# Optimization experiments

Measured on AMD Instinct MI355X. Metric: run time of the kernel, lower is better.

The kernel has to match this reference:

```python
import jax, jax.numpy as jnp
import numpy as np

N = 100000      # nodes
E = 1600000     # edges
F_IN = 512      # num_features
H = 128         # hidden
C = 40          # num_classes
K = 10          # Chebyshev order


def setup_inputs() -> dict:
    key = jax.random.key(0)
    ks = jax.random.split(key, 6)
    x = jax.random.normal(ks[0], (N, F_IN), dtype=jnp.float32)
    edge_index = jax.random.randint(ks[1], (2, E), 0, N, dtype=jnp.int32)
    W1 = jax.random.normal(ks[2], (F_IN, H), dtype=jnp.float32) / np.sqrt(F_IN).astype(np.float32)
    b1 = jnp.zeros((H,), dtype=jnp.float32)
    W2 = jax.random.normal(ks[3], (H, C), dtype=jnp.float32) / np.sqrt(H).astype(np.float32)
    b2 = jnp.zeros((C,), dtype=jnp.float32)
    # Chebyshev coefficients temp[K+1]
    temp = 1.0 + 0.1 * jax.random.normal(ks[4], (K + 1,), dtype=jnp.float32)
    return {"x": x, "edge_index": edge_index, "W1": W1, "b1": b1, "W2": W2, "b2": b2, "temp": temp}


def reference(x, edge_index, W1, b1, W2, b2, temp):
    # MLP encoder (eval mode: dropout is identity)
    h = jax.nn.relu(x @ W1 + b1)          # [N, H]
    h = h @ W2 + b2                        # [N, C]

    # gcn_norm: add self-loops, symmetric normalization
    self_loop = jnp.arange(N, dtype=edge_index.dtype)
    row = jnp.concatenate([edge_index[0], self_loop])   # [E+N]
    col = jnp.concatenate([edge_index[1], self_loop])
    deg = jax.ops.segment_sum(jnp.ones_like(row, dtype=jnp.float32), row, num_segments=N)
    dis = jnp.where(deg > 0, jax.lax.rsqrt(jnp.maximum(deg, 1.0)), 0.0)
    norm = dis[row] * dis[col]             # [E+N]

    def prop(v):  # A_hat @ v : gather-scale-scatter over edges
        return jax.ops.segment_sum(norm[:, None] * v[col], row, num_segments=N)

    # Chebyshev recurrence: Tx_k = 2*A_hat*Tx_{k-1} - Tx_{k-2}
    Tx0 = h
    Tx1 = prop(h)
    out0 = temp[0] * Tx0 + temp[1] * Tx1

    def body(carry, coe):
        t0, t1, acc = carry
        t2 = 2.0 * prop(t1) - t0
        return (t1, t2, acc + coe * t2), None

    (_, _, out), _ = jax.lax.scan(body, (Tx0, Tx1, out0), temp[2:])
    return jax.nn.log_softmax(out, axis=1)
```

## Files before the change

### kernel.cpp

```cpp
#include <hip/hip_runtime.h>
#include <hip/hip_bf16.h>
#include <cstdint>
#include <cstddef>

#define NN   100000
#define EE   1600000
#define FIN  512
#define HID  128
#define CC   40
#define KORD 10
#define SHB  80
#define SHSTRIDE ((size_t)NN * SHB)

typedef __attribute__((ext_vector_type(4))) float f4;
typedef __attribute__((ext_vector_type(8))) short short8_t;
typedef __attribute__((ext_vector_type(4))) unsigned int u4;
typedef __attribute__((ext_vector_type(4), aligned(4))) int i4u;

__device__ __forceinline__ unsigned short cvt_bf16(float f) {
  union { float f; unsigned u; } a; a.f = f;
  unsigned r = a.u + 0x7fffu + ((a.u >> 16) & 1u);
  return (unsigned short)(r >> 16);
}
__device__ __forceinline__ unsigned pk_bf(float a, float b) {
  union { float f; unsigned u; } x, y; x.f = a; y.f = b;
  unsigned ra = x.u + 0x7fffu + ((x.u >> 16) & 1u);
  unsigned rb = y.u + 0x7fffu + ((y.u >> 16) & 1u);
  return (ra >> 16) | (rb & 0xffff0000u);
}
__device__ __forceinline__ unsigned pk_tr(float a, float b) {
  union { float f; unsigned u; } x, y; x.f = a; y.f = b;
  return (x.u >> 16) | (y.u & 0xffff0000u);
}
__device__ __forceinline__ f4 cvf2(unsigned lo, unsigned hi) {
  union { unsigned u; float f; } a, b, c, d;
  a.u = lo << 16; b.u = lo & 0xffff0000u;
  c.u = hi << 16; d.u = hi & 0xffff0000u;
  f4 r; r.x = a.f; r.y = b.f; r.z = c.f; r.w = d.f; return r;
}

__global__ __launch_bounds__(256) void k_dw(const int* __restrict__ rowI, int* __restrict__ deg,
                                            const float* __restrict__ W1, unsigned short* __restrict__ W1T,
                                            int ndeg) {
  int b = blockIdx.x;
  if (b < ndeg) {
    int i = b * 256 + threadIdx.x;
    if (i < EE) atomicAdd(&deg[rowI[i]], 1);
  } else {
    int idx = (b - ndeg) * 256 + threadIdx.x;
    int k = idx >> 7, n = idx & 127;
    W1T[(k >> 5) * 4096 + n * 32 + (k & 31)] = cvt_bf16(W1[idx]);
  }
}

__global__ __launch_bounds__(256) void k_scan1(const int* __restrict__ cnt, int* __restrict__ excl,
                                               int* __restrict__ bsums) {
  __shared__ int s[256];
  int tid = threadIdx.x;
  int base = blockIdx.x * 1024 + tid * 4;
  int v0 = (base + 0 < NN) ? cnt[base + 0] + 1 : 0;
  int v1 = (base + 1 < NN) ? cnt[base + 1] + 1 : 0;
  int v2 = (base + 2 < NN) ? cnt[base + 2] + 1 : 0;
  int v3 = (base + 3 < NN) ? cnt[base + 3] + 1 : 0;
  int tsum = v0 + v1 + v2 + v3;
  s[tid] = tsum;
  __syncthreads();
  for (int off = 1; off < 256; off <<= 1) {
    int t = (tid >= off) ? s[tid - off] : 0;
    __syncthreads();
    if (tid >= off) s[tid] += t;
    __syncthreads();
  }
  int run = s[tid] - tsum;
  if (tid == 255) bsums[blockIdx.x] = s[255];
  if (base + 0 < NN) excl[base + 0] = run; run += v0;
  if (base + 1 < NN) excl[base + 1] = run; run += v1;
  if (base + 2 < NN) excl[base + 2] = run; run += v2;
  if (base + 3 < NN) excl[base + 3] = run;
}

__global__ __launch_bounds__(128) void k_scan2(int* __restrict__ bsums, int nb) {
  __shared__ int s[128];
  int tid = threadIdx.x;
  int v = (tid < nb) ? bsums[tid] : 0;
  s[tid] = v;
  __syncthreads();
  for (int off = 1; off < 128; off <<= 1) {
    int t = (tid >= off) ? s[tid - off] : 0;
    __syncthreads();
    if (tid >= off) s[tid] += t;
    __syncthreads();
  }
  if (tid < nb) bsums[tid] = s[tid] - v;
}

__global__ __launch_bounds__(256) void k_scan3(const int* __restrict__ cnt, int* __restrict__ rs,
                                               int* __restrict__ cur, const int* __restrict__ bsums,
                                               float* __restrict__ dis, float* __restrict__ sqd,
                                               float* __restrict__ invd) {
  int i = blockIdx.x * 256 + threadIdx.x;
  if (i < NN) {
    int v = rs[i] + bsums[i >> 10];
    rs[i] = v;
    cur[i] = v;
    int d = cnt[i] + 1;
    if (i == NN - 1) rs[NN] = v + d;
    float fd = (float)d;
    dis[i]  = rsqrtf(fd);
    sqd[i]  = sqrtf(fd);
    invd[i] = 1.0f / fd;
  }
}

#define SLICE_ROWS (NN / 8)
#define SC_CHUNK   2048
__global__ __launch_bounds__(256) void k_scatter(const int* __restrict__ rowI, const int* __restrict__ colI,
                                                 int* __restrict__ cur, int* __restrict__ colS) {
  int slice = blockIdx.x & 7;
  int chunk = blockIdx.x >> 3;
  int lo = slice * SLICE_ROWS, hi = lo + SLICE_ROWS;
#pragma unroll
  for (int t = 0; t < SC_CHUNK / 256; ++t) {
    int i = chunk * SC_CHUNK + t * 256 + threadIdx.x;
    if (i < EE + NN) {
      int r = (i < EE) ? rowI[i] : (i - EE);
      if (r >= lo && r < hi) {
        int c = (i < EE) ? colI[i] : r;
        int pos = atomicAdd(&cur[r], 1);
        colS[pos] = c * SHB;
      }
    }
  }
}

#define LDK 40
__global__ __launch_bounds__(256) void k_gemm1(const float* __restrict__ x, const unsigned short* __restrict__ W1T,
                                               const float* __restrict__ b1, float* __restrict__ h1) {
  __shared__ __align__(16) float As_f[128 * 32];
  __shared__ __align__(16) short Bs_s[128][LDK];
  int tid  = threadIdx.x;
  int wave = tid >> 6, lane = tid & 63;
  int blockRow = blockIdx.x * 128;
  int wr = (wave & 1) * 64, wc = (wave >> 1) * 64;
  int l15 = lane & 15, hi4 = lane >> 4;

  int sr = (wave << 5) + (lane >> 3);
  int sslot = lane & 7;

  f4 acc[4][4] = {};

  for (int k0 = 0; k0 < FIN; k0 += 32) {
#pragma unroll
    for (int c = 0; c < 4; ++c) {
      int row = sr + c * 8;
      int gr = blockRow + row;
      int lslot = sslot ^ (row & 7);
      const float* gp = x + (size_t)gr * FIN + k0 + lslot * 4;
      float* lp = &As_f[(wave << 10) + (c << 8)];
      if (gr < NN) {
        __builtin_amdgcn_global_load_lds(
            (const __attribute__((address_space(1))) unsigned int*)gp,
            (__attribute__((address_space(3))) unsigned int*)lp, 16, 0, 0);
      }
    }

    const unsigned short* Wt = W1T + (k0 >> 5) * 4096;
    short8_t q0 = *(const short8_t*)&Wt[tid * 16];
    short8_t q1 = *(const short8_t*)&Wt[tid * 16 + 8];
    int bn = tid >> 1, bkk = (tid & 1) * 16;
    *(short8_t*)&Bs_s[bn][bkk]     = q0;
    *(short8_t*)&Bs_s[bn][bkk + 8] = q1;

    __syncthreads();

    short8_t afr[4], bfr[4];
#pragma unroll
    for (int m = 0; m < 4; ++m) {
      int row = wr + m * 16 + l15;
      int s0 = (hi4 * 2) ^ (row & 7);
      int s1 = (hi4 * 2 + 1) ^ (row & 7);
      f4 a0 = *(const f4*)&As_f[(row << 5) + s0 * 4];
      f4 a1 = *(const f4*)&As_f[(row << 5) + s1 * 4];
      u4 p;
      p.x = pk_tr(a0.x, a0.y); p.y = pk_tr(a0.z, a0.w);
      p.z = pk_tr(a1.x, a1.y); p.w = pk_tr(a1.z, a1.w);
      afr[m] = *(short8_t*)&p;
    }
#pragma unroll
    for (int n = 0; n < 4; ++n) bfr[n] = *(const short8_t*)&Bs_s[wc + n * 16 + l15][hi4 * 8];
#pragma unroll
    for (int m = 0; m < 4; ++m)
#pragma unroll
      for (int n = 0; n < 4; ++n)
        acc[m][n] = __builtin_amdgcn_mfma_f32_16x16x32_bf16(afr[m], bfr[n], acc[m][n], 0, 0, 0);

    __syncthreads();
  }

  float bias[4];
#pragma unroll
  for (int n = 0; n < 4; ++n) bias[n] = b1[wc + n * 16 + l15];
#pragma unroll
  for (int m = 0; m < 4; ++m) {
    int baseRow = blockRow + wr + m * 16 + hi4 * 4;
#pragma unroll
    for (int n = 0; n < 4; ++n) {
      int col = wc + n * 16 + l15;
#pragma unroll
      for (int r = 0; r < 4; ++r) {
        int grow = baseRow + r;
        if (grow < NN) h1[(size_t)grow * HID + col] = fmaxf(acc[m][n][r] + bias[n], 0.f);
      }
    }
  }
}

__global__ __launch_bounds__(256) void k_gemm2(const float* __restrict__ h1, const float* __restrict__ W2,
                                               const float* __restrict__ b2, const float* __restrict__ temp,
                                               const float* __restrict__ dis,
                                               unsigned short* __restrict__ sh0) {
  __shared__ float sW[HID * CC];
  __shared__ float sb[CC];
  int tid = threadIdx.x;
  for (int i = tid; i < HID * CC; i += 256) sW[i] = W2[i];
  if (tid < CC) sb[tid] = b2[tid];
  __syncthreads();
  int gid = blockIdx.x * 256 + tid;
  if (gid >= NN * 20) return;
  int row = gid / 20;
  int c2  = (gid - row * 20) * 2;
  const float* hr = h1 + (size_t)row * HID;
  float a0 = sb[c2], a1 = sb[c2 + 1];
#pragma unroll 8
  for (int k = 0; k < HID; ++k) {
    float hv = hr[k];
    a0 = fmaf(hv, sW[k * CC + c2], a0);
    a1 = fmaf(hv, sW[k * CC + c2 + 1], a1);
  }
  float dv = dis[row];
  *(unsigned*)((char*)sh0 + (size_t)row * SHB + c2 * 2) = pk_bf(a0 * dv, a1 * dv);
}

template <int MODE>
__global__ __launch_bounds__(256) void k_prop(const unsigned short* __restrict__ shIn,
                                              const unsigned short* __restrict__ shPrev,
                                              unsigned short* __restrict__ shOut,
                                              const int* __restrict__ colS,
                                              const int* __restrict__ rs,
                                              const float* __restrict__ invd) {
  int lane = threadIdx.x & 63;
  int wave = threadIdx.x >> 6;
  int grp  = lane / 5;
  int fi   = lane - grp * 5;
  int node = blockIdx.x * 48 + wave * 12 + grp;
  bool active = (grp < 12) && (node < NN);
  int s = 0, e = 0;
  if (active) { s = rs[node]; e = rs[node + 1]; }
  const char* base = (const char*)shIn + fi * 16;
  f4 lo0 = {0.f,0.f,0.f,0.f}, hi0 = lo0, lo1 = lo0, hi1 = lo0;
  f4 lo2 = lo0, hi2 = lo0, lo3 = lo0, hi3 = lo0;
  int j = s;
  for (; j + 8 <= e; j += 8) {
    int c0 = colS[j],     c1 = colS[j + 1], c2 = colS[j + 2], c3 = colS[j + 3];
    int c4 = colS[j + 4], c5 = colS[j + 5], c6 = colS[j + 6], c7 = colS[j + 7];
    u4 p0 = *(const u4*)(base + c0);
    u4 p1 = *(const u4*)(base + c1);
    u4 p2 = *(const u4*)(base + c2);
    u4 p3 = *(const u4*)(base + c3);
    u4 p4 = *(const u4*)(base + c4);
    u4 p5 = *(const u4*)(base + c5);
    u4 p6 = *(const u4*)(base + c6);
    u4 p7 = *(const u4*)(base + c7);
    lo0 += cvf2(p0.x, p0.y); hi0 += cvf2(p0.z, p0.w);
    lo1 += cvf2(p1.x, p1.y); hi1 += cvf2(p1.z, p1.w);
    lo2 += cvf2(p2.x, p2.y); hi2 += cvf2(p2.z, p2.w);
    lo3 += cvf2(p3.x, p3.y); hi3 += cvf2(p3.z, p3.w);
    lo0 += cvf2(p4.x, p4.y); hi0 += cvf2(p4.z, p4.w);
    lo1 += cvf2(p5.x, p5.y); hi1 += cvf2(p5.z, p5.w);
    lo2 += cvf2(p6.x, p6.y); hi2 += cvf2(p6.z, p6.w);
    lo3 += cvf2(p7.x, p7.y); hi3 += cvf2(p7.z, p7.w);
  }
  if (j + 4 <= e) {
    int c0 = colS[j], c1 = colS[j + 1], c2 = colS[j + 2], c3 = colS[j + 3];
    u4 p0 = *(const u4*)(base + c0);
    u4 p1 = *(const u4*)(base + c1);
    u4 p2 = *(const u4*)(base + c2);
    u4 p3 = *(const u4*)(base + c3);
    lo0 += cvf2(p0.x, p0.y); hi0 += cvf2(p0.z, p0.w);
    lo1 += cvf2(p1.x, p1.y); hi1 += cvf2(p1.z, p1.w);
    lo2 += cvf2(p2.x, p2.y); hi2 += cvf2(p2.z, p2.w);
    lo3 += cvf2(p3.x, p3.y); hi3 += cvf2(p3.z, p3.w);
    j += 4;
  }
  if (j + 2 <= e) {
    u4 p0 = *(const u4*)(base + colS[j]);
    u4 p1 = *(const u4*)(base + colS[j + 1]);
    lo0 += cvf2(p0.x, p0.y); hi0 += cvf2(p0.z, p0.w);
    lo1 += cvf2(p1.x, p1.y); hi1 += cvf2(p1.z, p1.w);
    j += 2;
  }
  if (j < e) {
    u4 p0 = *(const u4*)(base + colS[j]);
    lo2 += cvf2(p0.x, p0.y); hi2 += cvf2(p0.z, p0.w);
  }

  if (active) {
    f4 slo = (lo0 + lo1) + (lo2 + lo3);
    f4 shi = (hi0 + hi1) + (hi2 + hi3);
    float iv = invd[node];
    size_t ro = (size_t)node * SHB + fi * 16;
    f4 wlo, whi;
    if (MODE == 0) {
      wlo = iv * slo; whi = iv * shi;
    } else {
      u4 pp = __builtin_nontemporal_load((const u4*)((const char*)shPrev + ro));
      f4 plo = cvf2(pp.x, pp.y), phi = cvf2(pp.z, pp.w);
      wlo = (2.f * iv) * slo - plo;
      whi = (2.f * iv) * shi - phi;
    }
    u4 pk;
    pk.x = pk_bf(wlo.x, wlo.y); pk.y = pk_bf(wlo.z, wlo.w);
    pk.z = pk_bf(whi.x, whi.y); pk.w = pk_bf(whi.z, whi.w);
    *(u4*)((char*)shOut + ro) = pk;
  }
}

__global__ __launch_bounds__(256) void k_comb(const unsigned short* __restrict__ shBase,
                                              float* __restrict__ outF,
                                              const float* __restrict__ sqd,
                                              const float* __restrict__ temp) {
  int lane = threadIdx.x & 63;
  int wave = threadIdx.x >> 6;
  int grp  = lane / 5;
  int fi   = lane - grp * 5;
  int node = blockIdx.x * 48 + wave * 12 + grp;
  if (grp >= 12 || node >= NN) return;

  const char* p = (const char*)shBase + (size_t)node * SHB + fi * 16;
  f4 alo = {0.f,0.f,0.f,0.f}, ahi = alo;
#pragma unroll
  for (int k = 0; k <= KORD; ++k) {
    u4 pp = *(const u4*)(p + (size_t)k * SHSTRIDE);
    float tk = temp[k];
    alo += tk * cvf2(pp.x, pp.y);
    ahi += tk * cvf2(pp.z, pp.w);
  }
  float sq = sqd[node];
  alo *= sq; ahi *= sq;

  int gb = grp * 5;
  float m = fmaxf(fmaxf(fmaxf(alo.x, alo.y), fmaxf(alo.z, alo.w)),
                  fmaxf(fmaxf(ahi.x, ahi.y), fmaxf(ahi.z, ahi.w)));
  float mm = m;
#pragma unroll
  for (int j = 0; j < 5; ++j) mm = fmaxf(mm, __shfl(m, gb + j));
  float ss = expf(alo.x - mm) + expf(alo.y - mm) + expf(alo.z - mm) + expf(alo.w - mm)
           + expf(ahi.x - mm) + expf(ahi.y - mm) + expf(ahi.z - mm) + expf(ahi.w - mm);
  float tot = 0.f;
#pragma unroll
  for (int j = 0; j < 5; ++j) tot += __shfl(ss, gb + j);
  float lse = mm + logf(tot);
  alo -= lse; ahi -= lse;
  size_t o = (size_t)node * CC + fi * 8;
  *(f4*)&outF[o]     = alo;
  *(f4*)&outF[o + 4] = ahi;
}

extern "C" void kernel_launch(void* const* d_in, const int* in_sizes, int n_in,
                              void* d_out, int out_size, void* d_ws, size_t ws_size,
                              hipStream_t stream) {
  const float* x    = (const float*)d_in[0];
  const int*   ei   = (const int*)d_in[1];
  const float* W1   = (const float*)d_in[2];
  const float* b1   = (const float*)d_in[3];
  const float* W2   = (const float*)d_in[4];
  const float* b2   = (const float*)d_in[5];
  const float* temp = (const float*)d_in[6];
  const int* rowI = ei;
  const int* colI = ei + EE;
  float* out = (float*)d_out;

  char* w = (char*)d_ws;
  auto alloc = [&](size_t bytes) -> void* {
    void* p = (void*)w;
    w += (bytes + 255) & ~(size_t)255;
    return p;
  };
  int*   deg   = (int*)  alloc((size_t)NN * 4);
  float* dis   = (float*)alloc((size_t)NN * 4);
  float* sqd   = (float*)alloc((size_t)NN * 4);
  float* invd  = (float*)alloc((size_t)NN * 4);
  int*   rs    = (int*)  alloc((size_t)(NN + 1) * 4);
  int*   cur   = (int*)  alloc((size_t)NN * 4);
  int*   bsums = (int*)  alloc(512 * 4);
  unsigned short* W1T = (unsigned short*)alloc((size_t)FIN * HID * 2);
  unsigned short* shAll = (unsigned short*)alloc(SHSTRIDE * (KORD + 1));
  int*   colS  = (int*)  alloc((size_t)(EE + NN) * 4);
  float* h1    = (float*)alloc((size_t)NN * HID * 4);

  auto sh = [&](int k) -> unsigned short* {
    return (unsigned short*)((char*)shAll + (size_t)k * SHSTRIDE);
  };

  hipMemsetAsync(deg, 0, (size_t)NN * 4, stream);

  const int NDEG = (EE + 255) / 256;
  const int NW1T = FIN * HID / 256;
  k_dw<<<NDEG + NW1T, 256, 0, stream>>>(rowI, deg, W1, W1T, NDEG);

  int nb = (NN + 1023) / 1024;
  k_scan1<<<nb, 256, 0, stream>>>(deg, rs, bsums);
  k_scan2<<<1, 128, 0, stream>>>(bsums, nb);
  k_scan3<<<(NN + 255) / 256, 256, 0, stream>>>(deg, rs, cur, bsums, dis, sqd, invd);

  const int NCH = (EE + NN + SC_CHUNK - 1) / SC_CHUNK;
  k_scatter<<<8 * NCH, 256, 0, stream>>>(rowI, colI, cur, colS);

  k_gemm1<<<(NN + 127) / 128, 256, 0, stream>>>(x, W1T, b1, h1);
  k_gemm2<<<(NN * 20 + 255) / 256, 256, 0, stream>>>(h1, W2, b2, temp, dis, sh(0));

  int G = (NN + 47) / 48;
  k_prop<0><<<G, 256, 0, stream>>>(sh(0), sh(0), sh(1), colS, rs, invd);
  for (int k = 2; k <= KORD; ++k) {
    k_prop<1><<<G, 256, 0, stream>>>(sh(k - 1), sh(k - 2), sh(k), colS, rs, invd);
  }

  k_comb<<<(NN + 47) / 48, 256, 0, stream>>>(shAll, out, sqd, temp);
}
```

Before: 627.6 us.

## Double-buffer GEMM1 A tiles per wave and load B fragments directly to registers

Rewrites the first MLP GEMM so each wave owns a private 32-row A tile in LDS, double-buffered with async global_load_lds. B fragments are loaded straight from global into registers instead of staged through shared memory. Block-wide __syncthreads are replaced by vmcnt/lgkmcnt waits, so the loads for the next k-step overlap the current MFMAs. The wave tiling changes from 64x64 to 32x128, and out-of-range rows are clamped rather than skipped. This relies on precise hand-written waitcnt counts and raises register use, since 16 B fragments are live at once.

```diff
diff --git a/kernel.cpp b/kernel.cpp
--- a/kernel.cpp
+++ b/kernel.cpp
@@ -133,79 +133,104 @@
   }
 }
 
-#define LDK 40
+#define NT1 (FIN / 32)
 __global__ __launch_bounds__(256) void k_gemm1(const float* __restrict__ x, const unsigned short* __restrict__ W1T,
                                                const float* __restrict__ b1, float* __restrict__ h1) {
-  __shared__ __align__(16) float As_f[128 * 32];
-  __shared__ __align__(16) short Bs_s[128][LDK];
+  __shared__ __align__(16) float As_f[4][2][1024];
   int tid  = threadIdx.x;
   int wave = tid >> 6, lane = tid & 63;
+  int l15 = lane & 15, hi4 = lane >> 4;
   int blockRow = blockIdx.x * 128;
-  int wr = (wave & 1) * 64, wc = (wave >> 1) * 64;
-  int l15 = lane & 15, hi4 = lane >> 4;
-
-  int sr = (wave << 5) + (lane >> 3);
+  int wrow = wave * 32;
+
+  int srl = lane >> 3;
   int sslot = lane & 7;
 
-  f4 acc[4][4] = {};
-
-  for (int k0 = 0; k0 < FIN; k0 += 32) {
+  f4 acc[2][8] = {};
+
+  auto issueA = [&](int t, int buf) {
+    int k0 = t * 32;
 #pragma unroll
     for (int c = 0; c < 4; ++c) {
-      int row = sr + c * 8;
-      int gr = blockRow + row;
-      int lslot = sslot ^ (row & 7);
+      int rl = c * 8 + srl;
+      int gr = blockRow + wrow + rl;
+      if (gr > NN - 1) gr = NN - 1;
+      int lslot = sslot ^ (rl & 7);
       const float* gp = x + (size_t)gr * FIN + k0 + lslot * 4;
-      float* lp = &As_f[(wave << 10) + (c << 8)];
-      if (gr < NN) {
-        __builtin_amdgcn_global_load_lds(
-            (const __attribute__((address_space(1))) unsigned int*)gp,
-            (__attribute__((address_space(3))) unsigned int*)lp, 16, 0, 0);
-      }
-    }
-
-    const unsigned short* Wt = W1T + (k0 >> 5) * 4096;
-    short8_t q0 = *(const short8_t*)&Wt[tid * 16];
-    short8_t q1 = *(const short8_t*)&Wt[tid * 16 + 8];
-    int bn = tid >> 1, bkk = (tid & 1) * 16;
-    *(short8_t*)&Bs_s[bn][bkk]     = q0;
-    *(short8_t*)&Bs_s[bn][bkk + 8] = q1;
-
-    __syncthreads();
-
-    short8_t afr[4], bfr[4];
-#pragma unroll
-    for (int m = 0; m < 4; ++m) {
-      int row = wr + m * 16 + l15;
-      int s0 = (hi4 * 2) ^ (row & 7);
-      int s1 = (hi4 * 2 + 1) ^ (row & 7);
-      f4 a0 = *(const f4*)&As_f[(row << 5) + s0 * 4];
-      f4 a1 = *(const f4*)&As_f[(row << 5) + s1 * 4];
+      float* lp = &As_f[wave][buf][c * 256];
+      __builtin_amdgcn_global_load_lds(
+          (const __attribute__((address_space(1))) unsigned int*)gp,
+          (__attribute__((address_space(3))) unsigned int*)lp, 16, 0, 0);
+    }
+  };
+  auto issueB = [&](int t, short8_t* B) {
+    const unsigned short* Wt = W1T + (size_t)t * 4096;
+#pragma unroll
+    for (int n = 0; n < 8; ++n)
+      B[n] = *(const short8_t*)&Wt[n * 512 + l15 * 32 + hi4 * 8];
+  };
+  auto compute = [&](int buf, short8_t* B) {
+    unsigned abase = (unsigned)(size_t)&As_f[wave][buf][0];
+    f4 a0, a1, a2, a3;
+    {
+      int rl = l15;
+      unsigned ad0 = abase + rl * 128 + (((hi4 * 2)     ^ (rl & 7)) * 16);
+      unsigned ad1 = abase + rl * 128 + (((hi4 * 2 + 1) ^ (rl & 7)) * 16);
+      asm volatile("ds_read_b128 %0, %1" : "=v"(a0) : "v"(ad0));
+      asm volatile("ds_read_b128 %0, %1" : "=v"(a1) : "v"(ad1));
+    }
+    {
+      int rl = 16 + l15;
+      unsigned ad0 = abase + rl * 128 + (((hi4 * 2)     ^ (rl & 7)) * 16);
+      unsigned ad1 = abase + rl * 128 + (((hi4 * 2 + 1) ^ (rl & 7)) * 16);
+      asm volatile("ds_read_b128 %0, %1" : "=v"(a2) : "v"(ad0));
+      asm volatile("ds_read_b128 %0, %1" : "=v"(a3) : "v"(ad1));
+    }
+    asm volatile("s_waitcnt lgkmcnt(0)" ::: "memory");
+    __builtin_amdgcn_sched_barrier(0);
+    short8_t afr0, afr1;
+    {
       u4 p;
       p.x = pk_tr(a0.x, a0.y); p.y = pk_tr(a0.z, a0.w);
       p.z = pk_tr(a1.x, a1.y); p.w = pk_tr(a1.z, a1.w);
-      afr[m] = *(short8_t*)&p;
-    }
-#pragma unroll
-    for (int n = 0; n < 4; ++n) bfr[n] = *(const short8_t*)&Bs_s[wc + n * 16 + l15][hi4 * 8];
-#pragma unroll
-    for (int m = 0; m < 4; ++m)
-#pragma unroll
-      for (int n = 0; n < 4; ++n)
-        acc[m][n] = __builtin_amdgcn_mfma_f32_16x16x32_bf16(afr[m], bfr[n], acc[m][n], 0, 0, 0);
-
-    __syncthreads();
-  }
-
-  float bias[4];
-#pragma unroll
-  for (int n = 0; n < 4; ++n) bias[n] = b1[wc + n * 16 + l15];
-#pragma unroll
-  for (int m = 0; m < 4; ++m) {
-    int baseRow = blockRow + wr + m * 16 + hi4 * 4;
-#pragma unroll
-    for (int n = 0; n < 4; ++n) {
-      int col = wc + n * 16 + l15;
+      afr0 = *(short8_t*)&p;
+      u4 q;
+      q.x = pk_tr(a2.x, a2.y); q.y = pk_tr(a2.z, a2.w);
+      q.z = pk_tr(a3.x, a3.y); q.w = pk_tr(a3.z, a3.w);
+      afr1 = *(short8_t*)&q;
+    }
+#pragma unroll
+    for (int n = 0; n < 8; ++n) {
+      acc[0][n] = __builtin_amdgcn_mfma_f32_16x16x32_bf16(afr0, B[n], acc[0][n], 0, 0, 0);
+      acc[1][n] = __builtin_amdgcn_mfma_f32_16x16x32_bf16(afr1, B[n], acc[1][n], 0, 0, 0);
+    }
+  };
+
+  short8_t B0[8], B1[8];
+  issueA(0, 0); issueB(0, B0);
+#pragma unroll
+  for (int t = 0; t < NT1; t += 2) {
+    int t1 = (t + 1) & (NT1 - 1);
+    int t2 = (t + 2) & (NT1 - 1);
+    issueA(t1, 1); issueB(t1, B1);
+    asm volatile("s_waitcnt vmcnt(12)" ::: "memory");
+    __builtin_amdgcn_sched_barrier(0);
+    compute(0, B0);
+    issueA(t2, 0); issueB(t2, B0);
+    asm volatile("s_waitcnt vmcnt(12)" ::: "memory");
+    __builtin_amdgcn_sched_barrier(0);
+    compute(1, B1);
+  }
+
+  float bias[8];
+#pragma unroll
+  for (int n = 0; n < 8; ++n) bias[n] = b1[n * 16 + l15];
+#pragma unroll
+  for (int m = 0; m < 2; ++m) {
+    int baseRow = blockRow + wrow + m * 16 + hi4 * 4;
+#pragma unroll
+    for (int n = 0; n < 8; ++n) {
+      int col = n * 16 + l15;
 #pragma unroll
       for (int r = 0; r < 4; ++r) {
         int grow = baseRow + r;
```

New measurement: 637.2 us. No clear change (+1.5%).
